# Performance work log

Measured on AMD Instinct MI355X. Metric: run time of the kernel, lower is better.

Reference implementation:

```python
import jax, jax.numpy as jnp
import numpy as np

N_HEAD = 2


def _time_encode(ts, freq, phase):
    # ts [N, L] -> [N, L, time_dim]; harmonic = cos(ts * basis_freq + phase)
    return jnp.cos(ts[..., None] * freq + phase)


def _layer_norm(x, g, b, eps=1e-5):
    m = jnp.mean(x, axis=-1, keepdims=True)
    v = jnp.mean((x - m) ** 2, axis=-1, keepdims=True)
    return (x - m) / jnp.sqrt(v + eps) * g + b


def _attn(src, src_t, ngh, ngh_t, mask, wq, wk, wv, fcw, fcb, lng, lnb, m1w, m1b, m2w, m2b):
    # TGAT AttnModel: src [N,h], src_t [N,1,h], ngh [N,K,h], ngh_t [N,K,h], mask [N,K] bool
    q = jnp.concatenate([src[:, None, :], src_t], axis=-1)  # [N,1,D], D=2h
    k = jnp.concatenate([ngh, ngh_t], axis=-1)              # [N,K,D]
    N, K, D = k.shape
    dk = D // N_HEAD
    qh = (q @ wq.T).reshape(N, 1, N_HEAD, dk)
    kh = (k @ wk.T).reshape(N, K, N_HEAD, dk)
    vh = (k @ wv.T).reshape(N, K, N_HEAD, dk)
    scores = jnp.einsum('nqhd,nkhd->nhqk', qh, kh) / jnp.sqrt(jnp.float32(dk))
    scores = jnp.where(mask[:, None, None, :], jnp.float32(-1e10), scores)
    a = jax.nn.softmax(scores, axis=-1)
    out = jnp.einsum('nhqk,nkhd->nqhd', a, vh).reshape(N, 1, D)
    out = out @ fcw.T + fcb
    out = _layer_norm(out + q, lng, lnb)[:, 0, :]  # residual + LN, squeeze query dim
    # MergeLayer: fc2(relu(fc1(cat[out, src])))
    h = jax.nn.relu(jnp.concatenate([out, src], axis=-1) @ m1w.T + m1b)
    return h @ m2w.T + m2b


def setup_inputs() -> dict:
    key = jax.random.key(0)
    ks = jax.random.split(key, 20)
    B, K, F, H = 2048, 20, 128, 128
    D, L, NAE, NNODE = 2 * H, 2, 4096, 100000
    s = 0.05
    n = lambda i, shape, sc=1.0: jax.random.normal(ks[i], shape, dtype=jnp.float32) * sc
    inp = {}
    inp['src_feat'] = n(0, (B, F))
    inp['src_t'] = jax.random.uniform(ks[1], (B,), jnp.float32, 0.0, 1000.0)
    inp['ngh1_idx'] = jax.random.randint(ks[2], (B, K), 0, NNODE)
    inp['ngh1_t'] = jax.random.uniform(ks[3], (B, K), jnp.float32, 0.0, 1000.0)
    inp['ngh1_feat'] = n(4, (B, K, F))
    inp['ngh2_idx'] = jax.random.randint(ks[5], (B * K, K), 0, NNODE)
    inp['ngh2_t'] = jax.random.uniform(ks[6], (B * K, K), jnp.float32, 0.0, 1000.0)
    inp['ngh2_feat'] = n(7, (B * K, K, F))
    inp['ae_x'] = n(8, (NAE, H))
    inp['ae_adj'] = jax.random.uniform(ks[9], (NAE, NAE), jnp.float32)
    inp['W_lin'] = n(10, (H, F), s)
    inp['b_lin'] = jnp.zeros((H,), jnp.float32)
    inp['basis_freq'] = (1.0 / 10 ** jnp.linspace(0.0, 9.0, H)).astype(jnp.float32)
    inp['phase'] = jnp.zeros((H,), jnp.float32)
    inp['attn_wq'] = n(11, (L, D, D), s)
    inp['attn_wk'] = n(12, (L, D, D), s)
    inp['attn_wv'] = n(13, (L, D, D), s)
    inp['attn_fc_w'] = n(14, (L, D, D), s)
    inp['attn_fc_b'] = jnp.zeros((L, D), jnp.float32)
    inp['attn_ln_g'] = jnp.ones((L, D), jnp.float32)
    inp['attn_ln_b'] = jnp.zeros((L, D), jnp.float32)
    inp['mrg_fc1_w'] = n(15, (L, H, D + H), s)
    inp['mrg_fc1_b'] = jnp.zeros((L, H), jnp.float32)
    inp['mrg_fc2_w'] = n(16, (L, H, H), s)
    inp['mrg_fc2_b'] = jnp.zeros((L, H), jnp.float32)
    inp['W_gc'] = n(17, (H, H), s)
    inp['b_gc'] = jnp.zeros((H,), jnp.float32)
    return inp


def reference(src_feat, src_t, ngh1_idx, ngh1_t, ngh1_feat, ngh2_idx, ngh2_t, ngh2_feat,
              ae_x, ae_adj, W_lin, b_lin, basis_freq, phase,
              attn_wq, attn_wk, attn_wv, attn_fc_w, attn_fc_b, attn_ln_g, attn_ln_b,
              mrg_fc1_w, mrg_fc1_b, mrg_fc2_w, mrg_fc2_b, W_gc, b_gc):
    B, K = ngh1_idx.shape
    BK = B * K
    lin = lambda x: x @ W_lin.T + b_lin
    te = lambda ts: _time_encode(ts, basis_freq, phase)
    ap = lambda i: (attn_wq[i], attn_wk[i], attn_wv[i], attn_fc_w[i], attn_fc_b[i],
                    attn_ln_g[i], attn_ln_b[i], mrg_fc1_w[i], mrg_fc1_b[i],
                    mrg_fc2_w[i], mrg_fc2_b[i])
    mask1 = ngh1_idx == 0
    mask2 = ngh2_idx == 0
    t0_B = te(jnp.zeros((B, 1), jnp.float32))
    t0_BK = te(jnp.zeros((BK, 1), jnp.float32))
    t1 = te(src_t[:, None] - ngh1_t)                         # [B,K,H]
    t2 = te(ngh1_t.reshape(BK)[:, None] - ngh2_t)            # [BK,K,H]
    # tem_conv(curr=2): layer-1 embeddings of src and its neighbors (attn layer 0)
    src_l1 = _attn(lin(src_feat), t0_B, lin(ngh1_feat), t1, mask1, *ap(0))    # [B,H]
    ngh_l1 = _attn(lin(ngh1_feat.reshape(BK, -1)), t0_BK, lin(ngh2_feat), t2, mask2, *ap(0))
    ngh_l1 = ngh_l1.reshape(B, K, -1)
    # top-level attention (attn layer 1)
    src_embed = _attn(src_l1, t0_B, ngh_l1, t1, mask1, *ap(1))                # [B,H]
    # GNN_SnapAuto autoencoder: GraphConvolution + sigmoid decode + MSE
    gc_z = ae_adj @ (ae_x @ W_gc) + b_gc
    recon_loss = jnp.mean((ae_adj - jax.nn.sigmoid(gc_z @ gc_z.T)) ** 2)
    return src_embed, recon_loss
```

## Files before the change

### kernel.cpp

```cpp
#include <hip/hip_runtime.h>
#include <math.h>


typedef _Float16 h2 __attribute__((ext_vector_type(2)));
typedef _Float16 h4 __attribute__((ext_vector_type(4)));
typedef _Float16 h8 __attribute__((ext_vector_type(8)));
typedef float f4 __attribute__((ext_vector_type(4)));


__global__ __launch_bounds__(256) void k_prep_a(
    const float* __restrict__ phase, const float* __restrict__ wq,
    const float* __restrict__ wk, const float* __restrict__ wvw,
    const float* __restrict__ Wlin, const float* __restrict__ blin,
    const float* __restrict__ m1w, const float* __restrict__ m2w,
    const float* __restrict__ Wgc,
    float* __restrict__ te0, float* __restrict__ cbf, float* __restrict__ Mb,
    float* __restrict__ OWa,
    _Float16* __restrict__ Wlinh, _Float16* __restrict__ m1wh,
    _Float16* __restrict__ m2wh, _Float16* __restrict__ WgcTh,
    float* __restrict__ lacc)
{
  __shared__ float te[128];
  __shared__ float bqv[128];
  int b = blockIdx.x, tid = threadIdx.x;

  if (b < 4) {
    int l = b >> 1, h = b & 1;
    if (tid < 128) {
      te[tid] = cosf(phase[tid]);
      if (b == 0) te0[tid] = te[tid];
    }
    __syncthreads();
    if (tid < 128) {
      const float* wr = wq + ((size_t)(l * 256 + h * 128 + tid)) * 256 + 128;
      float s = 0.f;
      for (int k = 0; k < 128; k++) s += wr[k] * te[k];
      bqv[tid] = s;
    }
    __syncthreads();
    {
      const float* wkb = wk + (size_t)l * 65536 + (size_t)h * 32768;
      float s = 0.f;
      for (int d = 0; d < 128; d++) s += wkb[(size_t)d * 256 + tid] * bqv[d];
      cbf[(l * 2 + h) * 256 + tid] = s;
    }
    return;
  }
  b -= 4;
  if (b < 512) {
    int lh = b >> 7, bx = b & 127;
    int l = lh >> 1, h = lh & 1;
    int idx = bx * 256 + tid;
    int e = idx >> 7, s = idx & 127;
    const float* wkb = wk + (size_t)l * 65536 + (size_t)h * 32768;
    const float* wqb = wq + (size_t)l * 65536 + (size_t)h * 32768;
    float acc = 0.f;
    for (int d = 0; d < 128; d++)
      acc += wkb[(size_t)d * 256 + e] * wqb[(size_t)d * 256 + s];
    Mb[(size_t)lh * 32768 + idx] = acc;
    return;
  }
  b -= 512;
  if (b < 780) {
    int ci = b / 260, bx = b % 260;
    int lyr = (ci == 2) ? 1 : 0;
    int ul  = (ci == 0) ? 1 : 0;
    float* OW = OWa + (size_t)ci * 2 * 128 * 260;
    const float* wvl = wvw + (size_t)lyr * 65536;
    int idx = bx * 256 + tid;
    int u = idx % 260; int d = (idx / 260) % 128; int h = idx / (260 * 128);
    const float* wr = wvl + (size_t)(h * 128 + d) * 256;
    float val = 0.f;
    if (u < 128) {
      if (ul) { for (int cc = 0; cc < 128; cc++) val += wr[cc] * Wlin[cc * 128 + u]; }
      else val = wr[u];
    } else if (u < 256) {
      val = wr[u];
    } else if (u == 256) {
      if (ul) { for (int cc = 0; cc < 128; cc++) val += wr[cc] * blin[cc]; }
    }
    OW[idx] = val;
    return;
  }
  b -= 780;
  {
    int idx = b * 256 + tid;
    if (idx == 0) lacc[0] = 0.f;
    int i = idx;
    if (i < 16384) { Wlinh[i] = (_Float16)Wlin[i]; return; }
    i -= 16384;
    if (i < 98304) { m1wh[i] = (_Float16)m1w[i]; return; }
    i -= 98304;
    if (i < 32768) { m2wh[i] = (_Float16)m2w[i]; return; }
    i -= 32768;
    {
      int c = i >> 7, r = i & 127;
      WgcTh[i] = (_Float16)Wgc[(size_t)r * 128 + c];
    }
  }
}


__global__ __launch_bounds__(256) void k_prep_b(
    const float* __restrict__ Mb, const float* __restrict__ cbf,
    const float* __restrict__ Wlin, const float* __restrict__ blin,
    const float* __restrict__ fcw, const float* __restrict__ OWa,
    _Float16* __restrict__ SWa, float* __restrict__ cba,
    _Float16* __restrict__ Fa)
{
  int b = blockIdx.x, tid = threadIdx.x;
  if (b < 780) {
    int ci = b / 260, bx = b % 260;
    int lyr = (ci == 2) ? 1 : 0;
    int ul  = (ci == 0) ? 1 : 0;
    const float* M2 = Mb + (size_t)lyr * 2 * 32768;
    const float* c2 = cbf + (size_t)lyr * 512;
    _Float16* SW = SWa + (size_t)ci * 520 * 128;
    float* cb = cba + (size_t)ci * 520;
    int idx = bx * 256 + tid;
    int urow = idx / 128, s = idx % 128;
    int h = urow / 260, u = urow % 260;
    const float* M = M2 + (size_t)h * 32768;
    const float* c = c2 + h * 256;
    float val = 0.f, cbv = 0.f;
    if (u < 128) {
      if (ul) {
        for (int cc = 0; cc < 128; cc++) {
          float w = Wlin[cc * 128 + u];
          val += w * M[cc * 128 + s];
          cbv += w * c[cc];
        }
      } else { val = M[u * 128 + s]; cbv = c[u]; }
    } else if (u < 256) {
      val = M[u * 128 + s]; cbv = c[u];
    } else if (u == 256) {
      if (ul) {
        for (int cc = 0; cc < 128; cc++) {
          float w = blin[cc];
          val += w * M[cc * 128 + s];
          cbv += w * c[cc];
        }
      }
    }
    SW[(size_t)urow * 128 + s] = (_Float16)val;
    if (s == 0) cb[urow] = cbv;
    return;
  }
  b -= 780;
  {
    int yy = b / 260, bx = b % 260;
    int ci = yy >> 1, h = yy & 1;
    int lyr = (ci == 2) ? 1 : 0;
    int idx = bx * 256 + tid;
    int p = idx / 260, u = idx % 260;
    const float* fw = fcw + (size_t)lyr * 65536 + (size_t)p * 256 + h * 128;
    const float* ow = OWa + (size_t)ci * 2 * 128 * 260 + (size_t)h * 128 * 260;
    float s = 0.f;
    for (int d = 0; d < 128; d++) s += fw[d] * ow[(size_t)d * 260 + u];
    Fa[(size_t)ci * 256 * 520 + (size_t)p * 520 + h * 260 + u] = (_Float16)s;
  }
}


struct GemmJob {
  const float* A; const _Float16* B; const float* bias; float* C;
  int lda, ldb, ldc, M, N, K, cmode, klen, gx, gy, nblk;
};

__device__ __forceinline__ void gemm128_body(int lb, const GemmJob& g) {
  __shared__ _Float16 As[128][72];
  __shared__ _Float16 Bs[128][72];
  int bx = lb % g.gx;
  int rest = lb / g.gx;
  int by = rest % g.gy;
  int z = rest / g.gy;

  int tid = threadIdx.x;
  int wv = tid >> 6, lane = tid & 63;
  int wm = wv >> 1, wn = wv & 1;
  int row0 = bx * 128, col0 = by * 128;
  int m0 = wm * 64, n0 = wn * 64;
  int lr = lane & 15, lk = lane >> 4;
  int kbeg = z * g.klen;
  int kend = kbeg + g.klen; if (kend > g.K) kend = g.K;

  f4 acc[4][4];
#pragma unroll
  for (int i = 0; i < 4; i++)
#pragma unroll
    for (int j = 0; j < 4; j++) acc[i][j] = (f4)0.f;

  int arow = tid >> 1;
  int acol = (tid & 1) * 32;
  int gar = row0 + arow;
  int gbr = col0 + arow;
  bool bvalid = gbr < g.N;

  for (int k0 = kbeg; k0 < kend; k0 += 64) {
    __syncthreads();
#pragma unroll
    for (int j = 0; j < 8; j++) {
      int ka = k0 + acol + j * 4;
      f4 v = (f4)0.f;
      if (ka < g.K) v = *(const f4*)&g.A[(size_t)gar * g.lda + ka];
      h4 hv = { (_Float16)v.x, (_Float16)v.y, (_Float16)v.z, (_Float16)v.w };
      *(h4*)&As[arow][acol + j * 4] = hv;
    }
#pragma unroll
    for (int j = 0; j < 8; j++) {
      int ka = k0 + acol + j * 4;
      h4 hv = (h4)(_Float16)0.f;
      if (bvalid && ka < g.K) hv = *(const h4*)&g.B[(size_t)gbr * g.ldb + ka];
      *(h4*)&Bs[arow][acol + j * 4] = hv;
    }
    __syncthreads();
#pragma unroll
    for (int kk = 0; kk < 2; kk++) {
      h8 af[4], bf[4];
#pragma unroll
      for (int i = 0; i < 4; i++)
        af[i] = *(h8*)&As[m0 + i * 16 + lr][kk * 32 + lk * 8];
#pragma unroll
      for (int j = 0; j < 4; j++)
        bf[j] = *(h8*)&Bs[n0 + j * 16 + lr][kk * 32 + lk * 8];
#pragma unroll
      for (int i = 0; i < 4; i++)
#pragma unroll
        for (int j = 0; j < 4; j++)
          acc[i][j] = __builtin_amdgcn_mfma_f32_16x16x32_f16(af[i], bf[j], acc[i][j], 0, 0, 0);
    }
  }
  float* Cz = g.C + (size_t)z * g.M * g.ldc;
#pragma unroll
  for (int j = 0; j < 4; j++) {
    int c = col0 + n0 + j * 16 + lr;
    if (c >= g.N) continue;
    float bz = (g.bias && z == 0) ? g.bias[c] : 0.f;
#pragma unroll
    for (int i = 0; i < 4; i++) {
      int rbase = row0 + m0 + i * 16 + lk * 4;
#pragma unroll
      for (int r = 0; r < 4; r++) {
        int rr = rbase + r;
        float v = acc[i][j][r] + bz;
        if (g.cmode == 0) Cz[(size_t)rr * g.ldc + c] = v;
        else if (g.cmode == 1) ((_Float16*)g.C)[(size_t)rr * g.ldc + c] = (_Float16)v;
        else ((_Float16*)g.C)[(size_t)c * g.ldc + rr] = (_Float16)v;
      }
    }
  }
}


struct UJob {
  const float* A; const _Float16* B; const float* bias; _Float16* C;
  int nblk;
};

__device__ __forceinline__ void ugemm_body(int lb, const UJob& g) {
  __shared__ _Float16 As[128][136];
  __shared__ _Float16 Bs[128][72];
  int tid = threadIdx.x;
  int wv = tid >> 6, lane = tid & 63;
  int wm = wv >> 1, wn = wv & 1;
  int row0 = lb * 128;
  int m0 = wm * 64, n0 = wn * 64;
  int lr = lane & 15, lk = lane >> 4;

  {
    int arow = tid >> 1;
    int acol = (tid & 1) * 64;
    const float* ap = &g.A[(size_t)(row0 + arow) * 128 + acol];
#pragma unroll
    for (int j = 0; j < 16; j++) {
      f4 v = *(const f4*)(ap + j * 4);
      h4 hv = { (_Float16)v.x, (_Float16)v.y, (_Float16)v.z, (_Float16)v.w };
      *(h4*)&As[arow][acol + j * 4] = hv;
    }
  }

  int brow = tid >> 1;
  int bcol = (tid & 1) * 32;
  for (int nt = 0; nt < 5; nt++) {
    int col0 = nt * 128;
    int gbr = col0 + brow;
    bool bvalid = gbr < 520;
    f4 acc[4][4];
#pragma unroll
    for (int i = 0; i < 4; i++)
#pragma unroll
      for (int j = 0; j < 4; j++) acc[i][j] = (f4)0.f;

#pragma unroll
    for (int kk2 = 0; kk2 < 2; kk2++) {
      int k0 = kk2 * 64;
      __syncthreads();
#pragma unroll
      for (int j = 0; j < 8; j++) {
        int ka = k0 + bcol + j * 4;
        h4 hv = (h4)(_Float16)0.f;
        if (bvalid) hv = *(const h4*)&g.B[(size_t)gbr * 128 + ka];
        *(h4*)&Bs[brow][bcol + j * 4] = hv;
      }
      __syncthreads();
#pragma unroll
      for (int kk = 0; kk < 2; kk++) {
        h8 af[4], bf[4];
#pragma unroll
        for (int i = 0; i < 4; i++)
          af[i] = *(h8*)&As[m0 + i * 16 + lr][k0 + kk * 32 + lk * 8];
#pragma unroll
        for (int j = 0; j < 4; j++)
          bf[j] = *(h8*)&Bs[n0 + j * 16 + lr][kk * 32 + lk * 8];
#pragma unroll
        for (int i = 0; i < 4; i++)
#pragma unroll
          for (int j = 0; j < 4; j++)
            acc[i][j] = __builtin_amdgcn_mfma_f32_16x16x32_f16(af[i], bf[j], acc[i][j], 0, 0, 0);
      }
    }
#pragma unroll
    for (int j = 0; j < 4; j++) {
      int c = col0 + n0 + j * 16 + lr;
      if (c >= 520) continue;
      float bz = g.bias[c];
#pragma unroll
      for (int i = 0; i < 4; i++) {
        int rbase = row0 + m0 + i * 16 + lk * 4;
#pragma unroll
        for (int r = 0; r < 4; r++)
          g.C[(size_t)(rbase + r) * 520 + c] = (_Float16)(acc[i][j][r] + bz);
      }
    }
  }
}

__global__ __launch_bounds__(256) void k_gemm_multi(
    GemmJob ja, GemmJob jb, GemmJob jc, const float* lacc, float* finout)
{
  int b = blockIdx.x;
  if (b < ja.nblk) { gemm128_body(b, ja); return; }
  b -= ja.nblk;
  if (b < jb.nblk) { gemm128_body(b, jb); return; }
  b -= jb.nblk;
  if (b < jc.nblk) { gemm128_body(b, jc); return; }
  if (finout && threadIdx.x == 0)
    finout[0] = lacc[0] * (1.0f / (4096.0f * 4096.0f));
}

__global__ __launch_bounds__(256) void k_l3(
    UJob ua, GemmJob jb, GemmJob jc)
{
  int b = blockIdx.x;
  if (b < ua.nblk) { ugemm_body(b, ua); return; }
  b -= ua.nblk;
  if (b < jb.nblk) { gemm128_body(b, jb); return; }
  b -= jb.nblk;
  if (b < jc.nblk) { gemm128_body(b, jc); return; }
}


struct ScoreJob {
  _Float16* UY; const float* feat; const float* tsrc; const float* tngh;
  const int* idx; int rows;
};

__device__ void score_body(int row, const ScoreJob& J,
                           const float* __restrict__ freq,
                           const float* __restrict__ phase)
{
  __shared__ _Float16 fsh[20][136];
  __shared__ _Float16 tesh[20][136];
  __shared__ _Float16 ush[544];
  __shared__ float fq[128], ph[128];
  __shared__ float ssh[2][20];
  __shared__ float ash[2][20];
  __shared__ float dtsh[20];
  __shared__ int   msh[20];
  int tid = threadIdx.x;
  _Float16* UY = J.UY;

  if (tid < 20) {
    dtsh[tid] = J.tsrc[row] - J.tngh[(size_t)row * 20 + tid];
    msh[tid] = (J.idx[(size_t)row * 20 + tid] == 0);
  }
  if (tid >= 128 && tid < 256) { fq[tid - 128] = freq[tid - 128]; ph[tid - 128] = phase[tid - 128]; }
  if (tid < 130) {
    h4 v = *(const h4*)&UY[(size_t)row * 520 + tid * 4];
    int p4 = (tid < 65) ? tid : tid + 1;
    *(h4*)&ush[p4 * 4] = v;
  }
  const float4* fg = (const float4*)(J.feat + (size_t)row * 2560);
  for (int i = tid; i < 640; i += 256) {
    int j = i >> 5, c4 = i & 31;
    float4 v = fg[i];
    h4 hv = { (_Float16)v.x, (_Float16)v.y, (_Float16)v.z, (_Float16)v.w };
    *(h4*)&fsh[j][c4 * 4] = hv;
  }
  __syncthreads();
  for (int i = tid; i < 2560; i += 256) {
    int j = i >> 7, t = i & 127;
    tesh[j][t] = (_Float16)__cosf(dtsh[j] * fq[t] + ph[t]);
  }
  __syncthreads();

  int g = tid >> 4, li = tid & 15;
#pragma unroll
  for (int it = 0; it < 3; it++) {
    int t = it * 16 + g;
    int valid = (t < 40);
    int h = valid ? (t / 20) : 0;
    int j = valid ? (t % 20) : 0;
    float part = 0.f;
    if (valid) {
      const _Float16* xp = (li < 8) ? &fsh[j][li * 16] : &tesh[j][(li - 8) * 16];
      const _Float16* up = &ush[h * 264 + li * 16];
#pragma unroll
      for (int e = 0; e < 8; e++) {
        h2 a = *(const h2*)(xp + e * 2);
        h2 b2 = *(const h2*)(up + e * 2);
        part = __builtin_amdgcn_fdot2(a, b2, part, false);
      }
    }
    for (int m = 8; m; m >>= 1) part += __shfl_xor(part, m, 16);
    if (valid && li == 0) ssh[h][j] = part + (float)ush[h * 264 + 256];
  }
  __syncthreads();

  if (tid < 64) {
    int head = tid >> 5, l2 = tid & 31;
    const float scale = 0.08838834764831845f;
    float s = (l2 < 20) ? (msh[l2] ? -1e10f : ssh[head][l2] * scale) : -3.0e38f;
    float mx = s;
    for (int m = 16; m; m >>= 1) mx = fmaxf(mx, __shfl_xor(mx, m, 32));
    float e = (l2 < 20) ? __expf(s - mx) : 0.f;
    float sum = e;
    for (int m = 16; m; m >>= 1) sum += __shfl_xor(sum, m, 32);
    if (l2 < 20) ash[head][l2] = e / sum;
  }
  __syncthreads();

  {
    int p = tid;
    const _Float16* colp = (p < 128) ? &fsh[0][p] : &tesh[0][p - 128];
    float a0 = 0.f, a1 = 0.f;
#pragma unroll 5
    for (int j = 0; j < 20; j++) {
      float x = (float)colp[j * 136];
      a0 += ash[0][j] * x;
      a1 += ash[1][j] * x;
    }
    UY[(size_t)row * 520 + p] = (_Float16)a0;
    UY[(size_t)row * 520 + 260 + p] = (_Float16)a1;
  }
  if (tid < 8) {
    int p = (tid < 4) ? (256 + tid) : (512 + tid);
    _Float16 v = (_Float16)((tid == 0 || tid == 4) ? 1.f : 0.f);
    UY[(size_t)row * 520 + p] = v;
  }
}

__global__ __launch_bounds__(256, 8) void k_score_multi(
    ScoreJob ja, ScoreJob jb, const float* __restrict__ freq,
    const float* __restrict__ phase,
    const float* __restrict__ zp, _Float16* __restrict__ zh, int nzb)
{
  int b = blockIdx.x;
  if (b < ja.rows) { score_body(b, ja, freq, phase); return; }
  b -= ja.rows;
  if (b < jb.rows) { score_body(b, jb, freq, phase); return; }
  b -= jb.rows;
  if (b < nzb) {
    int i = b * 256 + threadIdx.x;
    const f4* zp4 = (const f4*)zp;
    f4 s = (f4)0.f;
#pragma unroll
    for (int p = 0; p < 8; p++) {
      f4 v = zp4[(size_t)p * 131072 + i];
      s.x += v.x; s.y += v.y; s.z += v.z; s.w += v.w;
    }
    h4 o = { (_Float16)s.x, (_Float16)s.y, (_Float16)s.z, (_Float16)s.w };
    ((h4*)zh)[i] = o;
  }
}


struct TailJob {
  const _Float16* U; const _Float16* F; const float* fcb; const float* srcv;
  const float* lng; const float* lnb;
  const _Float16* m1w; const float* m1b;
  const _Float16* m2w; const float* m2b;
  float* outp; int nblk;
};

__device__ void tail_body(int blk, const TailJob& J, const float* __restrict__ te0)
{
  __shared__ _Float16 Ps[64][264];
  __shared__ _Float16 Ss[64][136];
  __shared__ float redS[64][4], redQ[64][4];
  __shared__ float mrow[64], rrow[64];
  int tid = threadIdx.x;
  int wv = tid >> 6, lane = tid & 63;
  int lr = lane & 15, lk = lane >> 4;
  int row0 = blk * 64;
  int n0 = wv * 64;

  {
    const float4* sg = (const float4*)(J.srcv + (size_t)row0 * 128);
    for (int i = tid; i < 2048; i += 256) {
      int rr = i >> 5, c4 = i & 31;
      float4 v = sg[i];
      h4 hv = { (_Float16)v.x, (_Float16)v.y, (_Float16)v.z, (_Float16)v.w };
      *(h4*)&Ss[rr][c4 * 4] = hv;
    }
  }

  f4 acc[4][4];
#pragma unroll
  for (int i = 0; i < 4; i++)
#pragma unroll
    for (int j = 0; j < 4; j++) acc[i][j] = (f4)0.f;
  for (int kt = 0; kt < 17; kt++) {
    int kb = kt * 32 + lk * 8;
    bool ok = (kb + 8 <= 520);
    h8 af[4], bf[4];
#pragma unroll
    for (int i = 0; i < 4; i++)
      af[i] = ok ? *(const h8*)&J.U[(size_t)(row0 + i * 16 + lr) * 520 + kb]
                 : (h8)(_Float16)0.f;
#pragma unroll
    for (int j = 0; j < 4; j++)
      bf[j] = ok ? *(const h8*)&J.F[(size_t)(n0 + j * 16 + lr) * 520 + kb]
                 : (h8)(_Float16)0.f;
#pragma unroll
    for (int i = 0; i < 4; i++)
#pragma unroll
      for (int j = 0; j < 4; j++)
        acc[i][j] = __builtin_amdgcn_mfma_f32_16x16x32_f16(af[i], bf[j], acc[i][j], 0, 0, 0);
  }

#pragma unroll
  for (int i = 0; i < 4; i++) {
#pragma unroll
    for (int r = 0; r < 4; r++) {
      int row_l = i * 16 + lk * 4 + r;
      float rs = 0.f, rq = 0.f;
#pragma unroll
      for (int j = 0; j < 4; j++) {
        int c = n0 + j * 16 + lr;
        float q = (c < 128) ? J.srcv[(size_t)(row0 + row_l) * 128 + c] : te0[c - 128];
        float v = acc[i][j][r] + J.fcb[c] + q;
        acc[i][j][r] = v;
        rs += v; rq += v * v;
      }
      for (int m = 8; m; m >>= 1) {
        rs += __shfl_xor(rs, m, 16);
        rq += __shfl_xor(rq, m, 16);
      }
      if (lr == 0) { redS[row_l][wv] = rs; redQ[row_l][wv] = rq; }
    }
  }
  __syncthreads();
  if (tid < 64) {
    float s4 = redS[tid][0] + redS[tid][1] + redS[tid][2] + redS[tid][3];
    float q4 = redQ[tid][0] + redQ[tid][1] + redQ[tid][2] + redQ[tid][3];
    float mean = s4 * (1.0f / 256.0f);
    float var = q4 * (1.0f / 256.0f) - mean * mean;
    mrow[tid] = mean;
    rrow[tid] = rsqrtf(var + 1e-5f);
  }
  __syncthreads();
#pragma unroll
  for (int i = 0; i < 4; i++) {
#pragma unroll
    for (int r = 0; r < 4; r++) {
      int row_l = i * 16 + lk * 4 + r;
      float mean = mrow[row_l], rstd = rrow[row_l];
#pragma unroll
      for (int j = 0; j < 4; j++) {
        int c = n0 + j * 16 + lr;
        Ps[row_l][c] = (_Float16)((acc[i][j][r] - mean) * rstd * J.lng[c] + J.lnb[c]);
      }
    }
  }
  __syncthreads();

  int wm = wv >> 1, wn = wv & 1;
  f4 a2[2][4];
#pragma unroll
  for (int i = 0; i < 2; i++)
#pragma unroll
    for (int j = 0; j < 4; j++) a2[i][j] = (f4)0.f;
  for (int kk = 0; kk < 12; kk++) {
    int kb = kk * 32 + lk * 8;
    h8 af[2], bf[4];
#pragma unroll
    for (int i = 0; i < 2; i++) {
      int rl = wm * 32 + i * 16 + lr;
      af[i] = (kb < 256) ? *(const h8*)&Ps[rl][kb] : *(const h8*)&Ss[rl][kb - 256];
    }
#pragma unroll
    for (int j = 0; j < 4; j++)
      bf[j] = *(const h8*)&J.m1w[(size_t)(wn * 64 + j * 16 + lr) * 384 + kb];
#pragma unroll
    for (int i = 0; i < 2; i++)
#pragma unroll
      for (int j = 0; j < 4; j++)
        a2[i][j] = __builtin_amdgcn_mfma_f32_16x16x32_f16(af[i], bf[j], a2[i][j], 0, 0, 0);
  }
  __syncthreads();
#pragma unroll
  for (int i = 0; i < 2; i++) {
#pragma unroll
    for (int j = 0; j < 4; j++) {
      int c = wn * 64 + j * 16 + lr;
      float bz = J.m1b[c];
#pragma unroll
      for (int r = 0; r < 4; r++) {
        float v = a2[i][j][r] + bz;
        if (v < 0.f) v = 0.f;
        Ss[wm * 32 + i * 16 + lk * 4 + r][c] = (_Float16)v;
      }
    }
  }
  __syncthreads();

  f4 a3[2][4];
#pragma unroll
  for (int i = 0; i < 2; i++)
#pragma unroll
    for (int j = 0; j < 4; j++) a3[i][j] = (f4)0.f;
#pragma unroll
  for (int kk = 0; kk < 4; kk++) {
    int kb = kk * 32 + lk * 8;
    h8 af[2], bf[4];
#pragma unroll
    for (int i = 0; i < 2; i++)
      af[i] = *(const h8*)&Ss[wm * 32 + i * 16 + lr][kb];
#pragma unroll
    for (int j = 0; j < 4; j++)
      bf[j] = *(const h8*)&J.m2w[(size_t)(wn * 64 + j * 16 + lr) * 128 + kb];
#pragma unroll
    for (int i = 0; i < 2; i++)
#pragma unroll
      for (int j = 0; j < 4; j++)
        a3[i][j] = __builtin_amdgcn_mfma_f32_16x16x32_f16(af[i], bf[j], a3[i][j], 0, 0, 0);
  }
#pragma unroll
  for (int j = 0; j < 4; j++) {
    int c = wn * 64 + j * 16 + lr;
    float bz = J.m2b[c];
#pragma unroll
    for (int i = 0; i < 2; i++) {
#pragma unroll
      for (int r = 0; r < 4; r++) {
        int rl = wm * 32 + i * 16 + lk * 4 + r;
        J.outp[(size_t)(row0 + rl) * 128 + c] = a3[i][j][r] + bz;
      }
    }
  }
}

__device__ void loss_body(int b, const _Float16* __restrict__ z,
                          const float* __restrict__ adj, float* __restrict__ acc)
{
  int bi = b & 31, bj = b >> 5;
  int tid = threadIdx.x;
  int wv = tid >> 6, lane = tid & 63;
  int wm = wv >> 1, wn = wv & 1;
  int lr = lane & 15, lk = lane >> 4;
  int row0 = bi * 128 + wm * 64;
  int col0 = bj * 128 + wn * 64;

  f4 accf[4][4];
#pragma unroll
  for (int i = 0; i < 4; i++)
#pragma unroll
    for (int j = 0; j < 4; j++) accf[i][j] = (f4)0.f;

#pragma unroll
  for (int kk = 0; kk < 4; kk++) {
    int ko = kk * 32 + lk * 8;
    h8 af[4], bf[4];
#pragma unroll
    for (int i = 0; i < 4; i++)
      af[i] = *(const h8*)&z[(size_t)(row0 + i * 16 + lr) * 128 + ko];
#pragma unroll
    for (int j = 0; j < 4; j++)
      bf[j] = *(const h8*)&z[(size_t)(col0 + j * 16 + lr) * 128 + ko];
#pragma unroll
    for (int i = 0; i < 4; i++)
#pragma unroll
      for (int j = 0; j < 4; j++)
        accf[i][j] = __builtin_amdgcn_mfma_f32_16x16x32_f16(af[i], bf[j], accf[i][j], 0, 0, 0);
  }

  float lsum = 0.f;
#pragma unroll
  for (int i = 0; i < 4; i++) {
    int rbase = row0 + i * 16 + lk * 4;
#pragma unroll
    for (int r = 0; r < 4; r++) {
      const float* arow = adj + (size_t)(rbase + r) * 4096;
#pragma unroll
      for (int j = 0; j < 4; j++) {
        float x = accf[i][j][r];
        float s = 1.0f / (1.0f + __expf(-x));
        float d = arow[col0 + j * 16 + lr] - s;
        lsum += d * d;
      }
    }
  }
  for (int m = 32; m; m >>= 1) lsum += __shfl_xor(lsum, m, 64);
  if (lane == 0) atomicAdd(acc, lsum);
}

__global__ __launch_bounds__(256) void k_tail_loss(
    TailJob ja, TailJob jb, const float* __restrict__ te0,
    const _Float16* __restrict__ z, const float* __restrict__ adj,
    float* __restrict__ lacc, int nloss)
{
  int b = blockIdx.x;
  if (b < ja.nblk) { tail_body(b, ja, te0); return; }
  b -= ja.nblk;
  if (b < jb.nblk) { tail_body(b, jb, te0); return; }
  b -= jb.nblk;
  if (b < nloss) loss_body(b, z, adj, lacc);
}


extern "C" void kernel_launch(void* const* d_in, const int* in_sizes, int n_in,
                              void* d_out, int out_size, void* d_ws, size_t ws_size,
                              hipStream_t stream) {
  const float* src_feat  = (const float*)d_in[0];
  const float* src_t     = (const float*)d_in[1];
  const int*   ngh1_idx  = (const int*)d_in[2];
  const float* ngh1_t    = (const float*)d_in[3];
  const float* ngh1_feat = (const float*)d_in[4];
  const int*   ngh2_idx  = (const int*)d_in[5];
  const float* ngh2_t    = (const float*)d_in[6];
  const float* ngh2_feat = (const float*)d_in[7];
  const float* ae_x      = (const float*)d_in[8];
  const float* ae_adj    = (const float*)d_in[9];
  const float* W_lin     = (const float*)d_in[10];
  const float* b_lin     = (const float*)d_in[11];
  const float* freq      = (const float*)d_in[12];
  const float* phase     = (const float*)d_in[13];
  const float* wq        = (const float*)d_in[14];
  const float* wk        = (const float*)d_in[15];
  const float* wvp       = (const float*)d_in[16];
  const float* fcw       = (const float*)d_in[17];
  const float* fcb       = (const float*)d_in[18];
  const float* lng       = (const float*)d_in[19];
  const float* lnb       = (const float*)d_in[20];
  const float* m1w       = (const float*)d_in[21];
  const float* m1b       = (const float*)d_in[22];
  const float* m2w       = (const float*)d_in[23];
  const float* m2b       = (const float*)d_in[24];
  const float* W_gc      = (const float*)d_in[25];
  const float* b_gc      = (const float*)d_in[26];
  float* out = (float*)d_out;

  const int NB = 2048, NA = 40960;

  char* w = (char*)d_ws;
  size_t off = 0;
  auto alloc = [&](size_t bytes) -> void* {
    void* p = (void*)(w + off);
    off += (bytes + 255) & ~(size_t)255;
    return p;
  };
  float* te0    = (float*)alloc(128 * 4);
  float* linS   = (float*)alloc((size_t)NB * 128 * 4);
  float* lin1   = (float*)alloc((size_t)NA * 128 * 4);
  float* src_l1 = (float*)alloc((size_t)NB * 128 * 4);
  float* ngh_l1 = (float*)alloc((size_t)NA * 128 * 4);
  float* Mb     = (float*)alloc((size_t)4 * 32768 * 4);
  float* cbf    = (float*)alloc(4 * 256 * 4);
  _Float16* SWh = (_Float16*)alloc((size_t)3 * 520 * 128 * 2);
  float* cbU    = (float*)alloc(3 * 520 * 4);
  float* OW     = (float*)alloc((size_t)3 * 2 * 128 * 260 * 4);
  _Float16* Fh  = (_Float16*)alloc((size_t)3 * 256 * 520 * 2);
  _Float16* Wlinh = (_Float16*)alloc(16384 * 2);
  _Float16* m1wh  = (_Float16*)alloc((size_t)2 * 128 * 384 * 2);
  _Float16* m2wh  = (_Float16*)alloc((size_t)2 * 128 * 128 * 2);
  _Float16* WgcTh = (_Float16*)alloc(16384 * 2);
  _Float16* xwTh  = (_Float16*)alloc((size_t)4096 * 128 * 2);
  float* zpart    = (float*)alloc((size_t)8 * 4096 * 128 * 4);
  _Float16* zh    = (_Float16*)alloc((size_t)4096 * 128 * 2);
  float* lacc     = (float*)alloc(256);
  _Float16* UbufA = (_Float16*)alloc((size_t)NA * 520 * 2);
  _Float16* UbufB = (_Float16*)alloc((size_t)NB * 520 * 2);
  _Float16* UbufC = (_Float16*)alloc((size_t)NB * 520 * 2);

  k_prep_a<<<1936, 256, 0, stream>>>(phase, wq, wk, wvp, W_lin, b_lin, m1w, m2w,
                                     W_gc, te0, cbf, Mb, OW, Wlinh, m1wh, m2wh,
                                     WgcTh, lacc);
  k_prep_b<<<2340, 256, 0, stream>>>(Mb, cbf, W_lin, b_lin, fcw, OW, SWh, cbU, Fh);

  GemmJob j0 = {};

  GemmJob jLinS = { src_feat,  Wlinh, b_lin,   linS,         128, 128, 128,
                    2048, 128, 128, 0, 128, 16, 1, 16 };
  GemmJob jLin1 = { ngh1_feat, Wlinh, b_lin,   lin1,         128, 128, 128,
                    40960, 128, 128, 0, 128, 320, 1, 320 };
  GemmJob jXwT  = { ae_x,      WgcTh, nullptr, (float*)xwTh, 128, 128, 4096,
                    4096, 128, 128, 2, 128, 32, 1, 32 };
  k_gemm_multi<<<368, 256, 0, stream>>>(jLinS, jLin1, jXwT, nullptr, nullptr);

  UJob uA = { lin1, SWh, cbU, UbufA, 320 };
  GemmJob jUB = { linS, SWh + 520 * 128,  cbU + 520, (float*)UbufB, 128, 128, 520,
                  2048, 520, 128, 1, 128, 16, 5, 80 };
  GemmJob jZB = { ae_adj, xwTh, b_gc, zpart, 4096, 4096, 128,
                  4096, 128, 4096, 0, 512, 32, 1, 256 };
  k_l3<<<320 + 80 + 256, 256, 0, stream>>>(uA, jUB, jZB);

  ScoreJob sA = { UbufA, ngh2_feat, ngh1_t, ngh2_t, ngh2_idx, NA };
  ScoreJob sB = { UbufB, lin1,      src_t,  ngh1_t, ngh1_idx, NB };
  k_score_multi<<<NA + NB + 512, 256, 0, stream>>>(sA, sB, freq, phase,
                                                   zpart, zh, 512);

  TailJob tA = { UbufA, Fh,             fcb, lin1, lng, lnb,
                 m1wh, m1b, m2wh, m2b, ngh_l1, NA / 64 };
  TailJob tB = { UbufB, Fh + 256 * 520, fcb, linS, lng, lnb,
                 m1wh, m1b, m2wh, m2b, src_l1, NB / 64 };
  k_tail_loss<<<NA / 64 + NB / 64 + 1024, 256, 0, stream>>>(
      tA, tB, te0, zh, ae_adj, lacc, 1024);

  GemmJob jUC = { src_l1, SWh + 2 * 520 * 128, cbU + 2 * 520, (float*)UbufC,
                  128, 128, 520, 2048, 520, 128, 1, 128, 16, 5, 80 };
  k_gemm_multi<<<81, 256, 0, stream>>>(jUC, j0, j0, lacc, out + (size_t)NB * 128);

  ScoreJob sC = { UbufC, ngh_l1, src_t, ngh1_t, ngh1_idx, NB };
  ScoreJob s0 = {};
  k_score_multi<<<NB, 256, 0, stream>>>(sC, s0, freq, phase, nullptr, nullptr, 0);

  TailJob tC = { UbufC, Fh + 2 * 256 * 520, fcb + 256, src_l1, lng + 256, lnb + 256,
                 m1wh + 128 * 384, m1b + 128, m2wh + 128 * 128, m2b + 128,
                 out, NB / 64 };
  TailJob t0 = {};
  k_tail_loss<<<NB / 64, 256, 0, stream>>>(tC, t0, te0, nullptr, nullptr,
                                           nullptr, 0);
}
```

Baseline: 464.0 us.

## Fuse linear GEMMs into prep_b and shrink tail shared memory for occupancy

The three input linear/xW GEMM jobs now run as extra blocks of k_prep_b, removing one kernel launch and letting them overlap with weight preparation. This is valid because they depend only on k_prep_a outputs. The tail kernel no longer stages src features into a separate shared buffer. It reads them from global memory and converts them on the fly, and it reuses one shared buffer for the LN output and the ReLU hidden. It also declares launch_bounds(256,3) to raise occupancy, in exchange for redundant global reads and possible register pressure.

```diff
diff --git a/kernel.cpp b/kernel.cpp
--- a/kernel.cpp
+++ b/kernel.cpp
@@ -101,12 +101,103 @@
 }
 
 
+struct GemmJob {
+  const float* A; const _Float16* B; const float* bias; float* C;
+  int lda, ldb, ldc, M, N, K, cmode, klen, gx, gy, nblk;
+};
+
+__device__ __forceinline__ void gemm128_body(int lb, const GemmJob& g) {
+  __shared__ _Float16 As[128][72];
+  __shared__ _Float16 Bs[128][72];
+  int bx = lb % g.gx;
+  int rest = lb / g.gx;
+  int by = rest % g.gy;
+  int z = rest / g.gy;
+
+  int tid = threadIdx.x;
+  int wv = tid >> 6, lane = tid & 63;
+  int wm = wv >> 1, wn = wv & 1;
+  int row0 = bx * 128, col0 = by * 128;
+  int m0 = wm * 64, n0 = wn * 64;
+  int lr = lane & 15, lk = lane >> 4;
+  int kbeg = z * g.klen;
+  int kend = kbeg + g.klen; if (kend > g.K) kend = g.K;
+
+  f4 acc[4][4];
+#pragma unroll
+  for (int i = 0; i < 4; i++)
+#pragma unroll
+    for (int j = 0; j < 4; j++) acc[i][j] = (f4)0.f;
+
+  int arow = tid >> 1;
+  int acol = (tid & 1) * 32;
+  int gar = row0 + arow;
+  int gbr = col0 + arow;
+  bool bvalid = gbr < g.N;
+
+  for (int k0 = kbeg; k0 < kend; k0 += 64) {
+    __syncthreads();
+#pragma unroll
+    for (int j = 0; j < 8; j++) {
+      int ka = k0 + acol + j * 4;
+      f4 v = (f4)0.f;
+      if (ka < g.K) v = *(const f4*)&g.A[(size_t)gar * g.lda + ka];
+      h4 hv = { (_Float16)v.x, (_Float16)v.y, (_Float16)v.z, (_Float16)v.w };
+      *(h4*)&As[arow][acol + j * 4] = hv;
+    }
+#pragma unroll
+    for (int j = 0; j < 8; j++) {
+      int ka = k0 + acol + j * 4;
+      h4 hv = (h4)(_Float16)0.f;
+      if (bvalid && ka < g.K) hv = *(const h4*)&g.B[(size_t)gbr * g.ldb + ka];
+      *(h4*)&Bs[arow][acol + j * 4] = hv;
+    }
+    __syncthreads();
+#pragma unroll
+    for (int kk = 0; kk < 2; kk++) {
+      h8 af[4], bf[4];
+#pragma unroll
+      for (int i = 0; i < 4; i++)
+        af[i] = *(h8*)&As[m0 + i * 16 + lr][kk * 32 + lk * 8];
+#pragma unroll
+      for (int j = 0; j < 4; j++)
+        bf[j] = *(h8*)&Bs[n0 + j * 16 + lr][kk * 32 + lk * 8];
+#pragma unroll
+      for (int i = 0; i < 4; i++)
+#pragma unroll
+        for (int j = 0; j < 4; j++)
+          acc[i][j] = __builtin_amdgcn_mfma_f32_16x16x32_f16(af[i], bf[j], acc[i][j], 0, 0, 0);
+    }
+  }
+  float* Cz = g.C + (size_t)z * g.M * g.ldc;
+#pragma unroll
+  for (int j = 0; j < 4; j++) {
+    int c = col0 + n0 + j * 16 + lr;
+    if (c >= g.N) continue;
+    float bz = (g.bias && z == 0) ? g.bias[c] : 0.f;
+#pragma unroll
+    for (int i = 0; i < 4; i++) {
+      int rbase = row0 + m0 + i * 16 + lk * 4;
+#pragma unroll
+      for (int r = 0; r < 4; r++) {
+        int rr = rbase + r;
+        float v = acc[i][j][r] + bz;
+        if (g.cmode == 0) Cz[(size_t)rr * g.ldc + c] = v;
+        else if (g.cmode == 1) ((_Float16*)g.C)[(size_t)rr * g.ldc + c] = (_Float16)v;
+        else ((_Float16*)g.C)[(size_t)c * g.ldc + rr] = (_Float16)v;
+      }
+    }
+  }
+}
+
+
 __global__ __launch_bounds__(256) void k_prep_b(
     const float* __restrict__ Mb, const float* __restrict__ cbf,
     const float* __restrict__ Wlin, const float* __restrict__ blin,
     const float* __restrict__ fcw, const float* __restrict__ OWa,
     _Float16* __restrict__ SWa, float* __restrict__ cba,
-    _Float16* __restrict__ Fa)
+    _Float16* __restrict__ Fa,
+    GemmJob j1, GemmJob j2, GemmJob j3)
 {
   int b = blockIdx.x, tid = threadIdx.x;
   if (b < 780) {
@@ -147,7 +238,7 @@
     return;
   }
   b -= 780;
-  {
+  if (b < 1560) {
     int yy = b / 260, bx = b % 260;
     int ci = yy >> 1, h = yy & 1;
     int lyr = (ci == 2) ? 1 : 0;
@@ -158,97 +249,14 @@
     float s = 0.f;
     for (int d = 0; d < 128; d++) s += fw[d] * ow[(size_t)d * 260 + u];
     Fa[(size_t)ci * 256 * 520 + (size_t)p * 520 + h * 260 + u] = (_Float16)s;
-  }
-}
-
-
-struct GemmJob {
-  const float* A; const _Float16* B; const float* bias; float* C;
-  int lda, ldb, ldc, M, N, K, cmode, klen, gx, gy, nblk;
-};
-
-__device__ __forceinline__ void gemm128_body(int lb, const GemmJob& g) {
-  __shared__ _Float16 As[128][72];
-  __shared__ _Float16 Bs[128][72];
-  int bx = lb % g.gx;
-  int rest = lb / g.gx;
-  int by = rest % g.gy;
-  int z = rest / g.gy;
-
-  int tid = threadIdx.x;
-  int wv = tid >> 6, lane = tid & 63;
-  int wm = wv >> 1, wn = wv & 1;
-  int row0 = bx * 128, col0 = by * 128;
-  int m0 = wm * 64, n0 = wn * 64;
-  int lr = lane & 15, lk = lane >> 4;
-  int kbeg = z * g.klen;
-  int kend = kbeg + g.klen; if (kend > g.K) kend = g.K;
-
-  f4 acc[4][4];
-#pragma unroll
-  for (int i = 0; i < 4; i++)
-#pragma unroll
-    for (int j = 0; j < 4; j++) acc[i][j] = (f4)0.f;
-
-  int arow = tid >> 1;
-  int acol = (tid & 1) * 32;
-  int gar = row0 + arow;
-  int gbr = col0 + arow;
-  bool bvalid = gbr < g.N;
-
-  for (int k0 = kbeg; k0 < kend; k0 += 64) {
-    __syncthreads();
-#pragma unroll
-    for (int j = 0; j < 8; j++) {
-      int ka = k0 + acol + j * 4;
-      f4 v = (f4)0.f;
-      if (ka < g.K) v = *(const f4*)&g.A[(size_t)gar * g.lda + ka];
-      h4 hv = { (_Float16)v.x, (_Float16)v.y, (_Float16)v.z, (_Float16)v.w };
-      *(h4*)&As[arow][acol + j * 4] = hv;
-    }
-#pragma unroll
-    for (int j = 0; j < 8; j++) {
-      int ka = k0 + acol + j * 4;
-      h4 hv = (h4)(_Float16)0.f;
-      if (bvalid && ka < g.K) hv = *(const h4*)&g.B[(size_t)gbr * g.ldb + ka];
-      *(h4*)&Bs[arow][acol + j * 4] = hv;
-    }
-    __syncthreads();
-#pragma unroll
-    for (int kk = 0; kk < 2; kk++) {
-      h8 af[4], bf[4];
-#pragma unroll
-      for (int i = 0; i < 4; i++)
-        af[i] = *(h8*)&As[m0 + i * 16 + lr][kk * 32 + lk * 8];
-#pragma unroll
-      for (int j = 0; j < 4; j++)
-        bf[j] = *(h8*)&Bs[n0 + j * 16 + lr][kk * 32 + lk * 8];
-#pragma unroll
-      for (int i = 0; i < 4; i++)
-#pragma unroll
-        for (int j = 0; j < 4; j++)
-          acc[i][j] = __builtin_amdgcn_mfma_f32_16x16x32_f16(af[i], bf[j], acc[i][j], 0, 0, 0);
-    }
-  }
-  float* Cz = g.C + (size_t)z * g.M * g.ldc;
-#pragma unroll
-  for (int j = 0; j < 4; j++) {
-    int c = col0 + n0 + j * 16 + lr;
-    if (c >= g.N) continue;
-    float bz = (g.bias && z == 0) ? g.bias[c] : 0.f;
-#pragma unroll
-    for (int i = 0; i < 4; i++) {
-      int rbase = row0 + m0 + i * 16 + lk * 4;
-#pragma unroll
-      for (int r = 0; r < 4; r++) {
-        int rr = rbase + r;
-        float v = acc[i][j][r] + bz;
-        if (g.cmode == 0) Cz[(size_t)rr * g.ldc + c] = v;
-        else if (g.cmode == 1) ((_Float16*)g.C)[(size_t)rr * g.ldc + c] = (_Float16)v;
-        else ((_Float16*)g.C)[(size_t)c * g.ldc + rr] = (_Float16)v;
-      }
-    }
-  }
+    return;
+  }
+  b -= 1560;
+  if (b < j1.nblk) { gemm128_body(b, j1); return; }
+  b -= j1.nblk;
+  if (b < j2.nblk) { gemm128_body(b, j2); return; }
+  b -= j2.nblk;
+  if (b < j3.nblk) { gemm128_body(b, j3); return; }
 }
 
 
@@ -495,8 +503,7 @@
 
 __device__ void tail_body(int blk, const TailJob& J, const float* __restrict__ te0)
 {
-  __shared__ _Float16 Ps[64][264];
-  __shared__ _Float16 Ss[64][136];
+  __shared__ _Float16 PsBuf[64 * 264];
   __shared__ float redS[64][4], redQ[64][4];
   __shared__ float mrow[64], rrow[64];
   int tid = threadIdx.x;
@@ -504,16 +511,6 @@
   int lr = lane & 15, lk = lane >> 4;
   int row0 = blk * 64;
   int n0 = wv * 64;
-
-  {
-    const float4* sg = (const float4*)(J.srcv + (size_t)row0 * 128);
-    for (int i = tid; i < 2048; i += 256) {
-      int rr = i >> 5, c4 = i & 31;
-      float4 v = sg[i];
-      h4 hv = { (_Float16)v.x, (_Float16)v.y, (_Float16)v.z, (_Float16)v.w };
-      *(h4*)&Ss[rr][c4 * 4] = hv;
-    }
-  }
 
   f4 acc[4][4];
 #pragma unroll
@@ -579,7 +576,8 @@
 #pragma unroll
       for (int j = 0; j < 4; j++) {
         int c = n0 + j * 16 + lr;
-        Ps[row_l][c] = (_Float16)((acc[i][j][r] - mean) * rstd * J.lng[c] + J.lnb[c]);
+        PsBuf[row_l * 264 + c] =
+            (_Float16)((acc[i][j][r] - mean) * rstd * J.lng[c] + J.lnb[c]);
       }
     }
   }
@@ -597,7 +595,15 @@
 #pragma unroll
     for (int i = 0; i < 2; i++) {
       int rl = wm * 32 + i * 16 + lr;
-      af[i] = (kb < 256) ? *(const h8*)&Ps[rl][kb] : *(const h8*)&Ss[rl][kb - 256];
+      if (kb < 256) {
+        af[i] = *(const h8*)&PsBuf[rl * 264 + kb];
+      } else {
+        const float* sp = &J.srcv[(size_t)(row0 + rl) * 128 + (kb - 256)];
+        f4 v0 = *(const f4*)sp;
+        f4 v1 = *(const f4*)(sp + 4);
+        af[i] = h8{ (_Float16)v0.x, (_Float16)v0.y, (_Float16)v0.z, (_Float16)v0.w,
+                    (_Float16)v1.x, (_Float16)v1.y, (_Float16)v1.z, (_Float16)v1.w };
+      }
     }
 #pragma unroll
     for (int j = 0; j < 4; j++)
@@ -619,7 +625,7 @@
       for (int r = 0; r < 4; r++) {
         float v = a2[i][j][r] + bz;
         if (v < 0.f) v = 0.f;
-        Ss[wm * 32 + i * 16 + lk * 4 + r][c] = (_Float16)v;
+        PsBuf[(wm * 32 + i * 16 + lk * 4 + r) * 136 + c] = (_Float16)v;
       }
     }
   }
@@ -636,7 +642,7 @@
     h8 af[2], bf[4];
 #pragma unroll
     for (int i = 0; i < 2; i++)
-      af[i] = *(const h8*)&Ss[wm * 32 + i * 16 + lr][kb];
+      af[i] = *(const h8*)&PsBuf[(wm * 32 + i * 16 + lr) * 136 + kb];
 #pragma unroll
     for (int j = 0; j < 4; j++)
       bf[j] = *(const h8*)&J.m2w[(size_t)(wn * 64 + j * 16 + lr) * 128 + kb];
@@ -715,7 +721,7 @@
   if (lane == 0) atomicAdd(acc, lsum);
 }
 
-__global__ __launch_bounds__(256) void k_tail_loss(
+__global__ __launch_bounds__(256, 3) void k_tail_loss(
     TailJob ja, TailJob jb, const float* __restrict__ te0,
     const _Float16* __restrict__ z, const float* __restrict__ adj,
     float* __restrict__ lacc, int nloss)
@@ -796,9 +802,6 @@
   k_prep_a<<<1936, 256, 0, stream>>>(phase, wq, wk, wvp, W_lin, b_lin, m1w, m2w,
                                      W_gc, te0, cbf, Mb, OW, Wlinh, m1wh, m2wh,
                                      WgcTh, lacc);
-  k_prep_b<<<2340, 256, 0, stream>>>(Mb, cbf, W_lin, b_lin, fcw, OW, SWh, cbU, Fh);
-
-  GemmJob j0 = {};
 
   GemmJob jLinS = { src_feat,  Wlinh, b_lin,   linS,         128, 128, 128,
                     2048, 128, 128, 0, 128, 16, 1, 16 };
@@ -806,7 +809,8 @@
                     40960, 128, 128, 0, 128, 320, 1, 320 };
   GemmJob jXwT  = { ae_x,      WgcTh, nullptr, (float*)xwTh, 128, 128, 4096,
                     4096, 128, 128, 2, 128, 32, 1, 32 };
-  k_gemm_multi<<<368, 256, 0, stream>>>(jLinS, jLin1, jXwT, nullptr, nullptr);
+  k_prep_b<<<2708, 256, 0, stream>>>(Mb, cbf, W_lin, b_lin, fcw, OW, SWh, cbU,
+                                     Fh, jLinS, jLin1, jXwT);
 
   UJob uA = { lin1, SWh, cbU, UbufA, 320 };
   GemmJob jUB = { linS, SWh + 520 * 128,  cbU + 520, (float*)UbufB, 128, 128, 520,
@@ -827,6 +831,7 @@
   k_tail_loss<<<NA / 64 + NB / 64 + 1024, 256, 0, stream>>>(
       tA, tB, te0, zh, ae_adj, lacc, 1024);
 
+  GemmJob j0 = {};
   GemmJob jUC = { src_l1, SWh + 2 * 520 * 128, cbU + 2 * 520, (float*)UbufC,
                   128, 128, 520, 2048, 520, 128, 1, 128, 16, 5, 80 };
   k_gemm_multi<<<81, 256, 0, stream>>>(jUC, j0, j0, lacc, out + (size_t)NB * 128);
```

Measured after the change: 483.6 us. 4.2% more time.
